# Kernel optimization log

Hardware: AMD Instinct MI355X
Metric: run time of the kernel (lower is better)

## Reference

```python
import jax, jax.numpy as jnp
import numpy as np
import math

B, T, F_ = 4, 1024, 1024
TO_DIM, FROM_DIM, LATENT, H = 1024, 1024, 1024, 16
HEAD_DIM = LATENT // H

def _linear_params(key, in_dim, out_dim):
    kw, kb = jax.random.split(key)
    bound = 1.0 / math.sqrt(in_dim)
    W = jax.random.uniform(kw, (out_dim, in_dim), minval=-bound, maxval=bound, dtype=jnp.float32)
    b = jax.random.uniform(kb, (out_dim,), minval=-bound, maxval=bound, dtype=jnp.float32)
    return W, b

def setup_inputs() -> dict:
    key = jax.random.key(0)
    ks = jax.random.split(key, 7)
    X_to = jax.random.normal(ks[0], (B, T, TO_DIM), dtype=jnp.float32)
    X_from = jax.random.normal(ks[1], (B, F_, FROM_DIM), dtype=jnp.float32)
    mask_from = jax.random.randint(ks[2], (B, T, F_), 0, 2, dtype=jnp.int32)
    Wq, bq = _linear_params(ks[3], TO_DIM, LATENT)
    Wk, bk = _linear_params(ks[4], FROM_DIM, LATENT)
    Wv, bv = _linear_params(ks[5], FROM_DIM, LATENT)
    Wo, bo = _linear_params(ks[6], LATENT, TO_DIM)
    return {"X_to": X_to, "X_from": X_from, "mask_from": mask_from,
            "Wq": Wq, "bq": bq, "Wk": Wk, "bk": bk, "Wv": Wv, "bv": bv, "Wo": Wo, "bo": bo}

def _split_heads(x):
    # [b, t, (h k)] -> [b, h, t, k]
    b, t, _ = x.shape
    return x.reshape(b, t, H, HEAD_DIM).transpose(0, 2, 1, 3)

def reference(X_to, X_from, mask_from, Wq, bq, Wk, bk, Wv, bv, Wo, bo):
    Q = _split_heads(X_to @ Wq.T + bq)
    # NOTE: source swaps names — K comes from v_linear, V from k_linear. Reproduced literally.
    K = _split_heads(X_from @ Wv.T + bv)
    V = _split_heads(X_from @ Wk.T + bk)
    attn = jnp.einsum('bhtk,bhfk->bhtf', Q, K) / math.sqrt(HEAD_DIM)
    attn = jnp.where(mask_from[:, None, :, :] == 0, jnp.float32(-10000.0), attn)
    attn = jax.nn.softmax(attn, axis=-1)
    out = jnp.einsum('bhtf,bhfk->bhtk', attn, V)  # [b,h,t,k]
    out = out.transpose(0, 2, 1, 3).reshape(X_to.shape[0], X_to.shape[1], LATENT)
    return out @ Wo.T + bo
```

## Files before the change

kernel.cpp:

```cpp
#include <hip/hip_runtime.h>
#include <hip/hip_bf16.h>
#include <math.h>

#define BB 4
#define TT 1024
#define FF 1024
#define DIM 1024
#define NH 16
#define HD 64
#define MROWS (BB * TT)
#define FB (FF / 64)

typedef __attribute__((ext_vector_type(8))) short short8;
typedef __attribute__((ext_vector_type(4))) short short4v;
typedef __attribute__((ext_vector_type(4))) float f32x4;
typedef __hip_bfloat16 bf16;

__device__ __forceinline__ void async_copy16(const void* g, void* l) {
    __builtin_amdgcn_global_load_lds((const __attribute__((address_space(1))) void*)g,
                                     (__attribute__((address_space(3))) void*)l,
                                     16, 0, 0);
}

#define BARRIER() __builtin_amdgcn_s_barrier()

struct ConvArgs {
    const float* src[6];
    bf16* dst[6];
    int nvec[6];
    int blk_end[6];
    const int* mask;
    unsigned long long* Mb;
};

__global__ __launch_bounds__(256) void convert_pack(ConvArgs a) {
    int bx = blockIdx.x;
    if (bx >= a.blk_end[5]) {
        const int lane = threadIdx.x & 63;
        const int waveId = (bx - a.blk_end[5]) * 4 + (threadIdx.x >> 6);
#pragma unroll
        for (int it = 0; it < 16; ++it) {
            int c = waveId * 16 + it;
            int v = a.mask[(size_t)c * 64 + lane];
            unsigned long long bits = __ballot(v != 0);
            if (lane == 0) a.Mb[c] = bits;
        }
        return;
    }
    int seg = 0;
#pragma unroll
    for (int k = 0; k < 5; ++k) if (bx >= a.blk_end[k]) seg = k + 1;
    int b0 = seg ? a.blk_end[seg - 1] : 0;
    int idx = (bx - b0) * 256 + threadIdx.x;
    if (idx >= a.nvec[seg]) return;
    float4 v = ((const float4*)a.src[seg])[idx];
    union { bf16 t[4]; ushort4 u; } o;
    o.t[0] = __float2bfloat16(v.x);
    o.t[1] = __float2bfloat16(v.y);
    o.t[2] = __float2bfloat16(v.z);
    o.t[3] = __float2bfloat16(v.w);
    *(ushort4*)(a.dst[seg] + 4 * (size_t)idx) = o.u;
}

#define BK 64

struct QkvArgs {
    const bf16* A[3]; const bf16* W[3]; const float* bias[3]; bf16* C[3];
    int N[3]; int biasRow[3]; float scale[3];
};

__global__ __launch_bounds__(256, 2) void gemm_qkv(QkvArgs q) {
    __shared__ bf16 lds[32768];

    const int op = blockIdx.z;
    const bf16* A = q.A[op];
    const bf16* W = q.W[op];
    const float* bias = q.bias[op];
    bf16* C = q.C[op];
    const int N = q.N[op];
    const int brow = q.biasRow[op];
    const float sc = q.scale[op];

    const int lin = blockIdx.x + 8 * blockIdx.y;
    const int xcd = lin & 7;
    const int t8  = lin >> 3;
    int m0, n0;
    if (brow) {
        m0 = (((t8 & 7) + xcd) & 7) * 128;
        n0 = (xcd * 4 + (t8 >> 3)) * 128;
    } else {
        m0 = (xcd * 4 + (t8 >> 3)) * 128;
        n0 = (((t8 & 7) + xcd) & 7) * 128;
    }

    const int tid  = threadIdx.x;
    const int lane = tid & 63;
    const int wave = tid >> 6;
    const int quad = lane >> 4;
    const int l16  = lane & 15;
    const int wm = wave & 1;
    const int wn = wave >> 1;
    const int wbase = tid & ~63;

    const int srow = tid >> 3;
    const int scol = (tid & 7) ^ (srow & 7);
    const bf16* pA = A + (size_t)(m0 + srow) * DIM + scol * 8;
    const bf16* pB = W + (size_t)(n0 + srow) * DIM + scol * 8;

#define STAGE(T) do { \
    const bf16* sa_ = pA + (size_t)(T) * 64; \
    const bf16* sb_ = pB + (size_t)(T) * 64; \
    bf16* base_ = lds + ((T) & 1) * 16384; \
    _Pragma("unroll") for (int j = 0; j < 4; ++j) { \
        async_copy16(sa_ + (size_t)(j * 32) * DIM, base_ + (j * 256 + wbase) * 8); \
        async_copy16(sb_ + (size_t)(j * 32) * DIM, base_ + 8192 + (j * 256 + wbase) * 8); \
    } \
} while (0)

    f32x4 acc[4][4] = {};

    STAGE(0); STAGE(1);
    asm volatile("s_waitcnt vmcnt(8)");
    BARRIER();

#pragma unroll 2
    for (int t = 0; t < 16; ++t) {
        const bf16* As = lds + (t & 1) * 16384;
        const bf16* Bs = As + 8192;

        short8 a2[2][4], b2[2][4];
#pragma unroll
        for (int kk = 0; kk < 2; ++kk) {
#pragma unroll
            for (int mi = 0; mi < 4; ++mi) {
                int r = wm * 64 + mi * 16 + l16;
                int p = (kk * 4 + quad) ^ (r & 7);
                a2[kk][mi] = *(const short8*)(As + r * 64 + p * 8);
            }
#pragma unroll
            for (int ni = 0; ni < 4; ++ni) {
                int r = wn * 64 + ni * 16 + l16;
                int p = (kk * 4 + quad) ^ (r & 7);
                b2[kk][ni] = *(const short8*)(Bs + r * 64 + p * 8);
            }
        }
        __builtin_amdgcn_s_setprio(1);
#pragma unroll
        for (int kk = 0; kk < 2; ++kk)
#pragma unroll
            for (int mi = 0; mi < 4; ++mi)
#pragma unroll
                for (int ni = 0; ni < 4; ++ni)
                    acc[mi][ni] = __builtin_amdgcn_mfma_f32_16x16x32_bf16(
                        a2[kk][mi], b2[kk][ni], acc[mi][ni], 0, 0, 0);
        __builtin_amdgcn_s_setprio(0);

        BARRIER();
        if (t + 2 < 16) STAGE(t + 2);
        if (t < 14)       { asm volatile("s_waitcnt vmcnt(8)"); }
        else if (t == 14) { asm volatile("s_waitcnt vmcnt(0)"); }
        BARRIER();
    }

    bf16* Cs = lds;
#pragma unroll
    for (int ni = 0; ni < 4; ++ni) {
        const int nl = wn * 64 + ni * 16 + l16;
        float bcol = brow ? 0.0f : bias[n0 + nl];
#pragma unroll
        for (int mi = 0; mi < 4; ++mi)
#pragma unroll
            for (int i = 0; i < 4; ++i) {
                const int ml = wm * 64 + mi * 16 + quad * 4 + i;
                float v = (acc[mi][ni][i] + (brow ? bias[m0 + ml] : bcol)) * sc;
                Cs[ml * 132 + nl] = __float2bfloat16(v);
            }
    }
    __syncthreads();
#pragma unroll
    for (int j = 0; j < 8; ++j) {
        int slot = j * 256 + tid;
        int rr = slot >> 4, cc = slot & 15;
        short8 v = *(const short8*)(Cs + rr * 132 + cc * 8);
        *(short8*)(C + (size_t)(m0 + rr) * N + n0 + cc * 8) = v;
    }
#undef STAGE
}

__global__ __launch_bounds__(256, 2) void gemm_o(
    const bf16* __restrict__ A, const bf16* __restrict__ W,
    const float* __restrict__ bias, float* __restrict__ C)
{
    __shared__ bf16 lds[24576];

    const int lin = blockIdx.x + 16 * blockIdx.y;
    const int xcd = lin & 7;
    const int t8  = lin >> 3;
    const int m0 = (xcd * 4 + (t8 >> 4)) * 128;
    const int n0 = (((t8 & 15) + 2 * xcd) & 15) * 64;

    const int tid  = threadIdx.x;
    const int lane = tid & 63;
    const int wave = tid >> 6;
    const int quad = lane >> 4;
    const int l16  = lane & 15;
    const int wm = wave & 1;
    const int wn = wave >> 1;
    const int wbase = tid & ~63;

    const int srow = tid >> 3;
    const int scol = (tid & 7) ^ (srow & 7);
    const bf16* pA = A + (size_t)(m0 + srow) * DIM + scol * 8;
    const bf16* pB = W + (size_t)(n0 + srow) * DIM + scol * 8;

#define STAGE_O(T) do { \
    const bf16* sa_ = pA + (size_t)(T) * 64; \
    const bf16* sb_ = pB + (size_t)(T) * 64; \
    bf16* ab_ = lds + ((T) & 1) * 8192; \
    bf16* bb_ = lds + 16384 + ((T) & 1) * 4096; \
    _Pragma("unroll") for (int j = 0; j < 4; ++j) \
        async_copy16(sa_ + (size_t)(j * 32) * DIM, ab_ + (j * 256 + wbase) * 8); \
    _Pragma("unroll") for (int j = 0; j < 2; ++j) \
        async_copy16(sb_ + (size_t)(j * 32) * DIM, bb_ + (j * 256 + wbase) * 8); \
} while (0)

    f32x4 acc[4][2] = {};

    STAGE_O(0); STAGE_O(1);
    asm volatile("s_waitcnt vmcnt(6)");
    BARRIER();

#pragma unroll 2
    for (int t = 0; t < 16; ++t) {
        const bf16* As = lds + (t & 1) * 8192;
        const bf16* Bs = lds + 16384 + (t & 1) * 4096;

        short8 a2[2][4], b2[2][2];
#pragma unroll
        for (int kk = 0; kk < 2; ++kk) {
#pragma unroll
            for (int mi = 0; mi < 4; ++mi) {
                int r = wm * 64 + mi * 16 + l16;
                int p = (kk * 4 + quad) ^ (r & 7);
                a2[kk][mi] = *(const short8*)(As + r * 64 + p * 8);
            }
#pragma unroll
            for (int ni = 0; ni < 2; ++ni) {
                int r = wn * 32 + ni * 16 + l16;
                int p = (kk * 4 + quad) ^ (r & 7);
                b2[kk][ni] = *(const short8*)(Bs + r * 64 + p * 8);
            }
        }
        __builtin_amdgcn_s_setprio(1);
#pragma unroll
        for (int kk = 0; kk < 2; ++kk)
#pragma unroll
            for (int mi = 0; mi < 4; ++mi)
#pragma unroll
                for (int ni = 0; ni < 2; ++ni)
                    acc[mi][ni] = __builtin_amdgcn_mfma_f32_16x16x32_bf16(
                        a2[kk][mi], b2[kk][ni], acc[mi][ni], 0, 0, 0);
        __builtin_amdgcn_s_setprio(0);

        BARRIER();
        if (t + 2 < 16) STAGE_O(t + 2);
        if (t < 14)       { asm volatile("s_waitcnt vmcnt(6)"); }
        else if (t == 14) { asm volatile("s_waitcnt vmcnt(0)"); }
        BARRIER();
    }

    float* Cs = (float*)lds;
#pragma unroll
    for (int ni = 0; ni < 2; ++ni) {
        const int nl = wn * 32 + ni * 16 + l16;
        const float bcol = bias[n0 + nl];
#pragma unroll
        for (int mi = 0; mi < 4; ++mi)
#pragma unroll
            for (int i = 0; i < 4; ++i) {
                const int ml = wm * 64 + mi * 16 + quad * 4 + i;
                Cs[ml * 66 + nl] = acc[mi][ni][i] + bcol;
            }
    }
    __syncthreads();
#pragma unroll
    for (int j = 0; j < 8; ++j) {
        int slot = j * 256 + tid;
        int rr = slot >> 4, cc = slot & 15;
        float4 v = *(const float4*)(Cs + rr * 66 + cc * 4);
        *(float4*)(C + (size_t)(m0 + rr) * DIM + n0 + cc * 4) = v;
    }
#undef STAGE_O
}

__global__ __launch_bounds__(256, 3) void attn_kernel(
    const bf16* Qg, const bf16* __restrict__ Kg, const bf16* __restrict__ Vtg,
    const unsigned long long* __restrict__ Mbits, bf16* Og)
{
    __shared__ bf16 Ks[2 * 64 * 64];
    __shared__ bf16 Vts[2 * 64 * 64];
    __shared__ bf16 Pt[64 * 72];
    __shared__ float ls[64];

    const int tid  = threadIdx.x;
    const int lane = tid & 63;
    const int wave = tid >> 6;
    const int quad = lane >> 4;
    const int l16  = lane & 15;

    const int lin = blockIdx.x + 16 * (blockIdx.y + 16 * blockIdx.z);
    const int xcd = lin & 7;
    const int t   = lin >> 3;
    const int bh  = xcd * 8 + (t >> 4);
    const int b   = bh >> 4;
    const int h   = bh & 15;
    const int t0  = (t & 15) * 64;

    const size_t qrow0 = (size_t)b * TT + t0;
    const size_t krow0 = (size_t)b * FF;
    const int wbase = tid & ~63;
    const int myrow = wave * 16 + l16;

    const bf16* qptr = Qg + (qrow0 + myrow) * DIM + h * HD;
    short8 qb0 = *(const short8*)(qptr + quad * 8);
    short8 qb1 = *(const short8*)(qptr + 32 + quad * 8);

    const int srow = tid >> 3;
    const int sg   = ((tid & 7) ^ (srow & 7)) * 8;
    const bf16* kS = Kg + (krow0 + srow) * DIM + h * HD + sg;
    const bf16* vS = Vtg + (size_t)(h * HD + srow) * MROWS + b * FF + sg;

#define STAGE_KV(BUF, IT) do { \
    const bf16* ks_ = kS + (size_t)((IT) * 64) * DIM; \
    const bf16* vs_ = vS + (IT) * 64; \
    bf16* kd_ = Ks + (BUF) * 4096 + wbase * 8; \
    bf16* vd_ = Vts + (BUF) * 4096 + wbase * 8; \
    async_copy16(ks_, kd_); \
    async_copy16(ks_ + (size_t)32 * DIM, kd_ + 2048); \
    async_copy16(vs_, vd_); \
    async_copy16(vs_ + (size_t)32 * MROWS, vd_ + 2048); \
} while (0)

    const unsigned long long* mrow = Mbits + (qrow0 + myrow) * FB;
    unsigned long long w = mrow[0];

    float lsum = 0.f;
    f32x4 oacc[4] = {};

    STAGE_KV(0, 0);
    STAGE_KV(1, 1);
    asm volatile("s_waitcnt vmcnt(4)");
    BARRIER();

#pragma unroll 2
    for (int it = 0; it < 16; ++it) {
        const bf16* Kc = Ks + (it & 1) * 4096;
        const bf16* Vc = Vts + (it & 1) * 4096;

        unsigned long long nw = (it < 15) ? mrow[it + 1] : 0;

        f32x4 sacc[4];
        __builtin_amdgcn_s_setprio(1);
#pragma unroll
        for (int ft = 0; ft < 4; ++ft) {
            int r = ft * 16 + l16;
            short8 ka0 = *(const short8*)(Kc + r * 64 + ((quad       ^ (r & 7)) * 8));
            short8 ka1 = *(const short8*)(Kc + r * 64 + (((quad + 4) ^ (r & 7)) * 8));
            f32x4 s = {};
            s = __builtin_amdgcn_mfma_f32_16x16x32_bf16(ka0, qb0, s, 0, 0, 0);
            s = __builtin_amdgcn_mfma_f32_16x16x32_bf16(ka1, qb1, s, 0, 0, 0);
            sacc[ft] = s;
        }
        __builtin_amdgcn_s_setprio(0);

#pragma unroll
        for (int ft = 0; ft < 4; ++ft) {
            const unsigned bits4 =
                (unsigned)(w >> (ft * 16 + quad * 4)) & 0xFu;
            union { short4v v; short s[4]; } pk;
            float psum = 0.f;
#pragma unroll
            for (int i = 0; i < 4; ++i) {
                float p = (bits4 >> i) & 1u ? __expf(sacc[ft][i]) : 0.f;
                psum += p;
                pk.s[i] = (short)__bfloat16_as_ushort(__float2bfloat16(p));
            }
            lsum += psum;
            *(short4v*)(Pt + myrow * 72 + ft * 16 + quad * 4) = pk.v;
        }
        w = nw;

        short8 pa[2];
        pa[0] = *(const short8*)(Pt + myrow * 72 + quad * 8);
        pa[1] = *(const short8*)(Pt + myrow * 72 + 32 + quad * 8);
        __builtin_amdgcn_s_setprio(1);
#pragma unroll
        for (int nt = 0; nt < 4; ++nt) {
            int rd = nt * 16 + l16;
#pragma unroll
            for (int kf = 0; kf < 2; ++kf) {
                int g = (kf * 4 + quad) ^ (rd & 7);
                short8 vb = *(const short8*)(Vc + rd * 64 + g * 8);
                oacc[nt] = __builtin_amdgcn_mfma_f32_16x16x32_bf16(pa[kf], vb, oacc[nt], 0, 0, 0);
            }
        }
        __builtin_amdgcn_s_setprio(0);

        BARRIER();
        if (it + 2 < 16) STAGE_KV(it & 1, it + 2);
        if (it < 14)       { asm volatile("s_waitcnt vmcnt(4)"); }
        else if (it == 14) { asm volatile("s_waitcnt vmcnt(0)"); }
        BARRIER();
    }
#undef STAGE_KV

    lsum += __shfl_xor(lsum, 16);
    lsum += __shfl_xor(lsum, 32);
    if (quad == 0) ls[myrow] = lsum;

#pragma unroll
    for (int i = 0; i < 4; ++i) {
        float inv = 1.0f / ls[wave * 16 + quad * 4 + i];
        const int prow = wave * 16 + quad * 4 + i;
#pragma unroll
        for (int nt = 0; nt < 4; ++nt)
            Pt[prow * 72 + nt * 16 + l16] = __float2bfloat16(oacc[nt][i] * inv);
    }
    __syncthreads();
#pragma unroll
    for (int j = 0; j < 2; ++j) {
        int s = j * 256 + tid;
        int rr = s >> 3, off = (s & 7) * 8;
        short8 v = *(const short8*)(Pt + rr * 72 + off);
        *(short8*)(Og + (qrow0 + rr) * DIM + h * HD + off) = v;
    }
}

extern "C" void kernel_launch(void* const* d_in, const int* in_sizes, int n_in,
                              void* d_out, int out_size, void* d_ws, size_t ws_size,
                              hipStream_t stream) {
    const float* X_to   = (const float*)d_in[0];
    const float* X_from = (const float*)d_in[1];
    const int*   mask   = (const int*)  d_in[2];
    const float* Wq     = (const float*)d_in[3];
    const float* bq     = (const float*)d_in[4];
    const float* Wk     = (const float*)d_in[5];
    const float* bk     = (const float*)d_in[6];
    const float* Wv     = (const float*)d_in[7];
    const float* bv     = (const float*)d_in[8];
    const float* Wo     = (const float*)d_in[9];
    const float* bo     = (const float*)d_in[10];
    float* out = (float*)d_out;

    char* ws = (char*)d_ws;
    bf16* Xt16 = (bf16*)(ws);
    bf16* Xf16 = (bf16*)(ws + (8u  << 20));
    bf16* Wq16 = (bf16*)(ws + (16u << 20));
    bf16* Wv16 = (bf16*)(ws + (18u << 20));
    bf16* Wk16 = (bf16*)(ws + (20u << 20));
    bf16* Wo16 = (bf16*)(ws + (22u << 20));
    bf16* Q16  = (bf16*)(ws + (24u << 20));
    bf16* K16  = (bf16*)(ws + (32u << 20));
    bf16* Vt16 = (bf16*)(ws + (40u << 20));
    unsigned long long* Mb = (unsigned long long*)(ws + (48u << 20));

    ConvArgs ca;
    ca.src[0] = X_to;   ca.dst[0] = Xt16; ca.nvec[0] = MROWS * DIM / 4;
    ca.src[1] = X_from; ca.dst[1] = Xf16; ca.nvec[1] = MROWS * DIM / 4;
    ca.src[2] = Wq;     ca.dst[2] = Wq16; ca.nvec[2] = DIM * DIM / 4;
    ca.src[3] = Wv;     ca.dst[3] = Wv16; ca.nvec[3] = DIM * DIM / 4;
    ca.src[4] = Wk;     ca.dst[4] = Wk16; ca.nvec[4] = DIM * DIM / 4;
    ca.src[5] = Wo;     ca.dst[5] = Wo16; ca.nvec[5] = DIM * DIM / 4;
    int cum = 0;
    for (int k = 0; k < 6; ++k) { cum += ca.nvec[k] / 256; ca.blk_end[k] = cum; }
    ca.mask = mask; ca.Mb = Mb;
    convert_pack<<<cum + 1024, 256, 0, stream>>>(ca);

    QkvArgs qa;
    qa.A[0] = Xt16; qa.W[0] = Wq16; qa.bias[0] = bq; qa.C[0] = Q16;
    qa.N[0] = DIM; qa.biasRow[0] = 0; qa.scale[0] = 0.125f;
    qa.A[1] = Xf16; qa.W[1] = Wv16; qa.bias[1] = bv; qa.C[1] = K16;
    qa.N[1] = DIM; qa.biasRow[1] = 0; qa.scale[1] = 1.0f;
    qa.A[2] = Wk16; qa.W[2] = Xf16; qa.bias[2] = bk; qa.C[2] = Vt16;
    qa.N[2] = MROWS; qa.biasRow[2] = 1; qa.scale[2] = 1.0f;
    gemm_qkv<<<dim3(8, 32, 3), 256, 0, stream>>>(qa);

    attn_kernel<<<dim3(TT / 64, NH, BB), 256, 0, stream>>>(
        Q16, K16, Vt16, Mb, Q16);

    gemm_o<<<dim3(DIM / 64, MROWS / 128), 256, 0, stream>>>(Q16, Wo16, bo, out);
}
```

Measured before the change: 219.5 us.

## Software-pipeline QK^T one tile ahead with triple-buffered K in attention kernel

Restructures the attention loop so the QK^T MFMAs for the next K tile are issued before the softmax/exp and PV work of the current tile, which lets matrix work overlap with the scalar exp and LDS traffic. K staging moves to a three-slot LDS ring fetched three tiles ahead, while V stays double-buffered two tiles ahead, and the vmcnt waits are adjusted to match. This adds 8KB of LDS and keeps extra score registers live, which may lower occupancy under the 3-blocks launch bound. The setprio hints around QK are dropped.

```diff
diff --git a/kernel.cpp b/kernel.cpp
--- a/kernel.cpp
+++ b/kernel.cpp
@@ -297,7 +297,7 @@
     const bf16* Qg, const bf16* __restrict__ Kg, const bf16* __restrict__ Vtg,
     const unsigned long long* __restrict__ Mbits, bf16* Og)
 {
-    __shared__ bf16 Ks[2 * 64 * 64];
+    __shared__ bf16 Ks[3 * 64 * 64];
     __shared__ bf16 Vts[2 * 64 * 64];
     __shared__ bf16 Pt[64 * 72];
     __shared__ float ls[64];
@@ -330,48 +330,57 @@
     const bf16* kS = Kg + (krow0 + srow) * DIM + h * HD + sg;
     const bf16* vS = Vtg + (size_t)(h * HD + srow) * MROWS + b * FF + sg;
 
-#define STAGE_KV(BUF, IT) do { \
+#define STAGE_K(SLOT, IT) do { \
     const bf16* ks_ = kS + (size_t)((IT) * 64) * DIM; \
-    const bf16* vs_ = vS + (IT) * 64; \
-    bf16* kd_ = Ks + (BUF) * 4096 + wbase * 8; \
-    bf16* vd_ = Vts + (BUF) * 4096 + wbase * 8; \
+    bf16* kd_ = Ks + (SLOT) * 4096 + wbase * 8; \
     async_copy16(ks_, kd_); \
     async_copy16(ks_ + (size_t)32 * DIM, kd_ + 2048); \
+} while (0)
+
+#define STAGE_V(SLOT, IT) do { \
+    const bf16* vs_ = vS + (IT) * 64; \
+    bf16* vd_ = Vts + (SLOT) * 4096 + wbase * 8; \
     async_copy16(vs_, vd_); \
     async_copy16(vs_ + (size_t)32 * MROWS, vd_ + 2048); \
 } while (0)
 
+#define QK_CLUSTER(DST, KPTR) do { \
+    _Pragma("unroll") for (int ft = 0; ft < 4; ++ft) { \
+        int r_ = ft * 16 + l16; \
+        short8 ka0 = *(const short8*)((KPTR) + r_ * 64 + ((quad       ^ (r_ & 7)) * 8)); \
+        short8 ka1 = *(const short8*)((KPTR) + r_ * 64 + (((quad + 4) ^ (r_ & 7)) * 8)); \
+        f32x4 s_ = {}; \
+        s_ = __builtin_amdgcn_mfma_f32_16x16x32_bf16(ka0, qb0, s_, 0, 0, 0); \
+        s_ = __builtin_amdgcn_mfma_f32_16x16x32_bf16(ka1, qb1, s_, 0, 0, 0); \
+        (DST)[ft] = s_; \
+    } \
+} while (0)
+
     const unsigned long long* mrow = Mbits + (qrow0 + myrow) * FB;
     unsigned long long w = mrow[0];
 
     float lsum = 0.f;
     f32x4 oacc[4] = {};
 
-    STAGE_KV(0, 0);
-    STAGE_KV(1, 1);
+    STAGE_K(0, 0); STAGE_K(1, 1); STAGE_V(0, 0);
+    STAGE_K(2, 2); STAGE_V(1, 1);
     asm volatile("s_waitcnt vmcnt(4)");
     BARRIER();
 
+    f32x4 scur[4];
+    QK_CLUSTER(scur, Ks);
+
 #pragma unroll 2
     for (int it = 0; it < 16; ++it) {
-        const bf16* Kc = Ks + (it & 1) * 4096;
         const bf16* Vc = Vts + (it & 1) * 4096;
 
         unsigned long long nw = (it < 15) ? mrow[it + 1] : 0;
 
-        f32x4 sacc[4];
-        __builtin_amdgcn_s_setprio(1);
-#pragma unroll
-        for (int ft = 0; ft < 4; ++ft) {
-            int r = ft * 16 + l16;
-            short8 ka0 = *(const short8*)(Kc + r * 64 + ((quad       ^ (r & 7)) * 8));
-            short8 ka1 = *(const short8*)(Kc + r * 64 + (((quad + 4) ^ (r & 7)) * 8));
-            f32x4 s = {};
-            s = __builtin_amdgcn_mfma_f32_16x16x32_bf16(ka0, qb0, s, 0, 0, 0);
-            s = __builtin_amdgcn_mfma_f32_16x16x32_bf16(ka1, qb1, s, 0, 0, 0);
-            sacc[ft] = s;
+        f32x4 snxt[4] = {};
+        if (it < 15) {
+            const bf16* Kn = Ks + ((it + 1) % 3) * 4096;
+            QK_CLUSTER(snxt, Kn);
         }
-        __builtin_amdgcn_s_setprio(0);
 
 #pragma unroll
         for (int ft = 0; ft < 4; ++ft) {
@@ -381,7 +390,7 @@
             float psum = 0.f;
 #pragma unroll
             for (int i = 0; i < 4; ++i) {
-                float p = (bits4 >> i) & 1u ? __expf(sacc[ft][i]) : 0.f;
+                float p = (bits4 >> i) & 1u ? __expf(scur[ft][i]) : 0.f;
                 psum += p;
                 pk.s[i] = (short)__bfloat16_as_ushort(__float2bfloat16(p));
             }
@@ -407,12 +416,19 @@
         __builtin_amdgcn_s_setprio(0);
 
         BARRIER();
-        if (it + 2 < 16) STAGE_KV(it & 1, it + 2);
-        if (it < 14)       { asm volatile("s_waitcnt vmcnt(4)"); }
+        if (it + 3 < 16) STAGE_K((it + 3) % 3, it + 3);
+        if (it + 2 < 16) STAGE_V((it + 2) & 1, it + 2);
+        if (it < 13)       { asm volatile("s_waitcnt vmcnt(4)"); }
+        else if (it == 13) { asm volatile("s_waitcnt vmcnt(2)"); }
         else if (it == 14) { asm volatile("s_waitcnt vmcnt(0)"); }
         BARRIER();
-    }
-#undef STAGE_KV
+
+        scur[0] = snxt[0]; scur[1] = snxt[1];
+        scur[2] = snxt[2]; scur[3] = snxt[3];
+    }
+#undef STAGE_K
+#undef STAGE_V
+#undef QK_CLUSTER
 
     lsum += __shfl_xor(lsum, 16);
     lsum += __shfl_xor(lsum, 32);
```

Measured after the change: 216.0 us. No clear change (-1.6%).
